# Kernel optimization log

Hardware: AMD Instinct MI355X
Metric: run time of the kernel (lower is better)

## Reference

```python
import jax, jax.numpy as jnp
import numpy as np

N_NODES = 50000
N_EDGES = 800000
D_IN = 128
D_OUT = 128


def setup_inputs() -> dict:
    key = jax.random.key(0)
    k = jax.random.split(key, 6)
    x = jax.random.normal(k[0], (N_NODES, D_IN), dtype=jnp.float32)
    weight = jax.random.normal(k[1], (D_IN, D_OUT), dtype=jnp.float32) * (1.0 / np.sqrt(D_IN))
    bias = jax.random.normal(k[2], (D_OUT,), dtype=jnp.float32)
    src = jax.random.randint(k[3], (N_EDGES,), 0, N_NODES, dtype=jnp.int32)
    dst = jax.random.randint(k[4], (N_EDGES,), 0, N_NODES, dtype=jnp.int32)
    edge_vals = jax.random.uniform(k[5], (N_EDGES,), dtype=jnp.float32)
    return {"x": x, "weight": weight, "bias": bias, "src": src, "dst": dst, "edge_vals": edge_vals}


def reference(x, weight, bias, src, dst, edge_vals):
    # support = x @ W  (dense projection), [N, D_OUT]
    support = jnp.matmul(x, weight)
    # spmm: out[d] = sum_{e: dst[e]==d} edge_vals[e] * support[src[e]]
    msgs = support[src] * edge_vals[:, None]  # [E, D_OUT]
    out = jax.ops.segment_sum(msgs, dst, num_segments=x.shape[0])
    return out + bias
```

## Files before the change

### kernel.cpp

```cpp
#include <hip/hip_runtime.h>
#include <hip/hip_bf16.h>

#define D 128
#define BKT 64
#define CAP 1536
#define SC_EPB 4096
#define NBMAX 800

typedef __attribute__((ext_vector_type(8))) short bf16x8;
typedef __attribute__((ext_vector_type(4))) float f32x4;

__device__ __forceinline__ unsigned short f2bf(float f) {
  union { float f; unsigned u; } c; c.f = f;
  unsigned u = c.u + 0x7FFFu + ((c.u >> 16) & 1u);
  return (unsigned short)(u >> 16);
}
__device__ __forceinline__ float bf_lo(unsigned u) {
  union { unsigned u; float f; } c; c.u = u << 16; return c.f;
}
__device__ __forceinline__ float bf_hi(unsigned u) {
  union { unsigned u; float f; } c; c.u = u & 0xFFFF0000u; return c.f;
}

__global__ __launch_bounds__(256) void setup(
    const float* __restrict__ w, unsigned short* __restrict__ wT,
    int* __restrict__ bcur, int nb) {
  const int idx = blockIdx.x * 256 + threadIdx.x;
  if (idx < D * D) {
    const int k = idx >> 7, n = idx & 127;
    wT[n * D + k] = f2bf(w[idx]);
  }
  if (idx < nb) bcur[idx] = 0;
}

__global__ __launch_bounds__(256) void gemm_xw_mfma(
    const float* __restrict__ x, const unsigned short* __restrict__ wT,
    unsigned short* __restrict__ supb, int n_nodes) {
  __shared__ unsigned short xs[64 * 136];

  const int tid = threadIdx.x;
  const int row0 = blockIdx.x * 64;

  for (int f = tid; f < 64 * 32; f += 256) {
    const int r = f >> 5, c4 = f & 31;
    const int gr = row0 + r;
    float4 v = make_float4(0.f, 0.f, 0.f, 0.f);
    if (gr < n_nodes) v = ((const float4*)(x + (size_t)gr * D))[c4];
    ushort4 b;
    b.x = f2bf(v.x); b.y = f2bf(v.y); b.z = f2bf(v.z); b.w = f2bf(v.w);
    *(ushort4*)(&xs[r * 136 + c4 * 4]) = b;
  }
  __syncthreads();

  const int wv = tid >> 6;
  const int lane = tid & 63;
  const int l15 = lane & 15;
  const int quad = lane >> 4;

  f32x4 acc[8];
#pragma unroll
  for (int t = 0; t < 8; t++) acc[t] = (f32x4){0.f, 0.f, 0.f, 0.f};

#pragma unroll
  for (int k0 = 0; k0 < D; k0 += 32) {
    const bf16x8 a = *(const bf16x8*)(&xs[(wv * 16 + l15) * 136 + k0 + quad * 8]);
    const unsigned short* wp = wT + (size_t)l15 * D + k0 + quad * 8;
#pragma unroll
    for (int t = 0; t < 8; t++) {
      const bf16x8 b = *(const bf16x8*)(wp + (size_t)t * 16 * D);
      acc[t] = __builtin_amdgcn_mfma_f32_16x16x32_bf16(a, b, acc[t], 0, 0, 0);
    }
  }

#pragma unroll
  for (int t = 0; t < 8; t++) {
    const int col = t * 16 + l15;
#pragma unroll
    for (int r = 0; r < 4; r++) {
      const int row = row0 + wv * 16 + quad * 4 + r;
      if (row < n_nodes) supb[(size_t)row * D + col] = f2bf(acc[t][r]);
    }
  }
}

__global__ __launch_bounds__(512) void bucket_scatter(
    const int* __restrict__ src, const int* __restrict__ dst,
    const float* __restrict__ ev, int* __restrict__ bcur,
    uint2* __restrict__ staged, int n_edges, int nb) {
  __shared__ int hist[NBMAX];
  __shared__ int cur[NBMAX];
  const int t = threadIdx.x;
  const int base = blockIdx.x * SC_EPB;
  const int cnt = min(SC_EPB, n_edges - base);

  for (int i = t; i < nb; i += 512) hist[i] = 0;
  __syncthreads();
  for (int j = t; j < cnt; j += 512) atomicAdd(&hist[dst[base + j] >> 6], 1);
  __syncthreads();
  for (int i = t; i < nb; i += 512) {
    const int h = hist[i];
    cur[i] = h ? atomicAdd(&bcur[i], h) : 0;
  }
  __syncthreads();
  for (int j = t; j < cnt; j += 512) {
    const int e = base + j;
    const int d = dst[e];
    const int b = d >> 6;
    const int p = atomicAdd(&cur[b], 1);
    if (p < CAP) {
      staged[(size_t)b * CAP + p] =
          make_uint2((unsigned)src[e] | ((unsigned)(d & 63) << 16),
                     (unsigned)__float_as_int(ev[e]));
    }
  }
}

__global__ __launch_bounds__(1024) void bucket_reduce(
    const unsigned short* __restrict__ supb, const uint2* __restrict__ staged,
    const int* __restrict__ bcnt, const float* __restrict__ bias,
    float* __restrict__ out, int n_nodes) {
  __shared__ uint2 rec[CAP];
  __shared__ uint2 ordered[CAP];
  __shared__ int hist[BKT];
  __shared__ int segbase[BKT];
  __shared__ int cur[BKT];

  const int t = threadIdx.x;
  const int b = blockIdx.x;
  const int lo = b << 6;
  const int cnt = min(bcnt[b], CAP);
  const uint2* st = staged + (size_t)b * CAP;

  if (t < BKT) hist[t] = 0;
  __syncthreads();
  for (int j = t; j < cnt; j += 1024) {
    const uint2 p = st[j];
    rec[j] = p;
    atomicAdd(&hist[p.x >> 16], 1);
  }
  __syncthreads();
  if (t < BKT) {
    const int h = hist[t];
    int incl = h;
#pragma unroll
    for (int ofs = 1; ofs < 64; ofs <<= 1) {
      const int v = __shfl_up(incl, ofs, 64);
      if (t >= ofs) incl += v;
    }
    segbase[t] = incl - h;
    cur[t] = incl - h;
  }
  __syncthreads();
  for (int j = t; j < cnt; j += 1024) {
    const uint2 p = rec[j];
    const int pos = atomicAdd(&cur[p.x >> 16], 1);
    ordered[pos] = p;
  }
  __syncthreads();

  const int n = t >> 4;
  const int p = t & 15;
  const int beg = segbase[n];
  const int end = beg + hist[n];

  float a[8];
#pragma unroll
  for (int k = 0; k < 8; k++) a[k] = 0.f;

  int j = beg;
  for (; j + 2 <= end; j += 2) {
    const uint2 pr0 = ordered[j];
    const uint2 pr1 = ordered[j + 1];
    const uint4 r0 = ((const uint4*)(supb + (size_t)(pr0.x & 0xFFFF) * D))[p];
    const uint4 r1 = ((const uint4*)(supb + (size_t)(pr1.x & 0xFFFF) * D))[p];
    const float v0 = __int_as_float((int)pr0.y);
    const float v1 = __int_as_float((int)pr1.y);
    a[0] += v0 * bf_lo(r0.x) + v1 * bf_lo(r1.x);
    a[1] += v0 * bf_hi(r0.x) + v1 * bf_hi(r1.x);
    a[2] += v0 * bf_lo(r0.y) + v1 * bf_lo(r1.y);
    a[3] += v0 * bf_hi(r0.y) + v1 * bf_hi(r1.y);
    a[4] += v0 * bf_lo(r0.z) + v1 * bf_lo(r1.z);
    a[5] += v0 * bf_hi(r0.z) + v1 * bf_hi(r1.z);
    a[6] += v0 * bf_lo(r0.w) + v1 * bf_lo(r1.w);
    a[7] += v0 * bf_hi(r0.w) + v1 * bf_hi(r1.w);
  }
  if (j < end) {
    const uint2 pr0 = ordered[j];
    const uint4 r0 = ((const uint4*)(supb + (size_t)(pr0.x & 0xFFFF) * D))[p];
    const float v0 = __int_as_float((int)pr0.y);
    a[0] += v0 * bf_lo(r0.x);
    a[1] += v0 * bf_hi(r0.x);
    a[2] += v0 * bf_lo(r0.y);
    a[3] += v0 * bf_hi(r0.y);
    a[4] += v0 * bf_lo(r0.z);
    a[5] += v0 * bf_hi(r0.z);
    a[6] += v0 * bf_lo(r0.w);
    a[7] += v0 * bf_hi(r0.w);
  }

  const int node = lo + n;
  if (node < n_nodes) {
    const float4 bv0 = ((const float4*)bias)[p * 2];
    const float4 bv1 = ((const float4*)bias)[p * 2 + 1];
    float4* op = (float4*)out + (size_t)node * 32 + p * 2;
    op[0] = make_float4(a[0] + bv0.x, a[1] + bv0.y, a[2] + bv0.z, a[3] + bv0.w);
    op[1] = make_float4(a[4] + bv1.x, a[5] + bv1.y, a[6] + bv1.z, a[7] + bv1.w);
  }
}

extern "C" void kernel_launch(void* const* d_in, const int* in_sizes, int n_in,
                              void* d_out, int out_size, void* d_ws, size_t ws_size,
                              hipStream_t stream) {
  const float* x    = (const float*)d_in[0];
  const float* w    = (const float*)d_in[1];
  const float* bias = (const float*)d_in[2];
  const int*   src  = (const int*)d_in[3];
  const int*   dst  = (const int*)d_in[4];
  const float* ev   = (const float*)d_in[5];
  float* out = (float*)d_out;

  const int n_nodes = in_sizes[0] / D;
  const int n_edges = in_sizes[3];
  const int nb = (n_nodes + BKT - 1) / BKT;

  unsigned short* supb = (unsigned short*)d_ws;
  unsigned short* wT = supb + (size_t)n_nodes * D;
  int* bcur = (int*)(wT + D * D);
  uint2* staged = (uint2*)(bcur + NBMAX);

  setup<<<64, 256, 0, stream>>>(w, wT, bcur, nb);

  bucket_scatter<<<(n_edges + SC_EPB - 1) / SC_EPB, 512, 0, stream>>>(
      src, dst, ev, bcur, staged, n_edges, nb);

  gemm_xw_mfma<<<(n_nodes + 63) / 64, 256, 0, stream>>>(x, wT, supb, n_nodes);

  bucket_reduce<<<nb, 1024, 0, stream>>>(supb, staged, bcur, bias, out, n_nodes);
}
```

Measured before the change: 153.0 us.

## Fuse edge bucket scatter and GEMM into one launch; unroll reduce by four

Merges the edge-bucketing scatter kernel and the bf16 MFMA projection GEMM into a single launch, with the block index range split between the two roles. The independent scatter and GEMM work can then run concurrently on the GPU, and one kernel launch and the idle gap between the two kernels disappear. GEMM blocks now hold two 64-row sub-tiles of 256 threads each, which doubles the block's shared memory. The reduce loop's gather is also unrolled from two to four edges per iteration to raise memory-level parallelism, at the cost of more registers.

```diff
diff --git a/kernel.cpp b/kernel.cpp
--- a/kernel.cpp
+++ b/kernel.cpp
@@ -33,84 +33,87 @@
   if (idx < nb) bcur[idx] = 0;
 }
 
-__global__ __launch_bounds__(256) void gemm_xw_mfma(
+__global__ __launch_bounds__(512) void fused_scatter_gemm(
     const float* __restrict__ x, const unsigned short* __restrict__ wT,
-    unsigned short* __restrict__ supb, int n_nodes) {
-  __shared__ unsigned short xs[64 * 136];
-
-  const int tid = threadIdx.x;
-  const int row0 = blockIdx.x * 64;
-
-  for (int f = tid; f < 64 * 32; f += 256) {
-    const int r = f >> 5, c4 = f & 31;
-    const int gr = row0 + r;
-    float4 v = make_float4(0.f, 0.f, 0.f, 0.f);
-    if (gr < n_nodes) v = ((const float4*)(x + (size_t)gr * D))[c4];
-    ushort4 b;
-    b.x = f2bf(v.x); b.y = f2bf(v.y); b.z = f2bf(v.z); b.w = f2bf(v.w);
-    *(ushort4*)(&xs[r * 136 + c4 * 4]) = b;
-  }
-  __syncthreads();
-
-  const int wv = tid >> 6;
-  const int lane = tid & 63;
-  const int l15 = lane & 15;
-  const int quad = lane >> 4;
-
-  f32x4 acc[8];
-#pragma unroll
-  for (int t = 0; t < 8; t++) acc[t] = (f32x4){0.f, 0.f, 0.f, 0.f};
-
-#pragma unroll
-  for (int k0 = 0; k0 < D; k0 += 32) {
-    const bf16x8 a = *(const bf16x8*)(&xs[(wv * 16 + l15) * 136 + k0 + quad * 8]);
-    const unsigned short* wp = wT + (size_t)l15 * D + k0 + quad * 8;
-#pragma unroll
-    for (int t = 0; t < 8; t++) {
-      const bf16x8 b = *(const bf16x8*)(wp + (size_t)t * 16 * D);
-      acc[t] = __builtin_amdgcn_mfma_f32_16x16x32_bf16(a, b, acc[t], 0, 0, 0);
-    }
-  }
-
-#pragma unroll
-  for (int t = 0; t < 8; t++) {
-    const int col = t * 16 + l15;
-#pragma unroll
-    for (int r = 0; r < 4; r++) {
-      const int row = row0 + wv * 16 + quad * 4 + r;
-      if (row < n_nodes) supb[(size_t)row * D + col] = f2bf(acc[t][r]);
-    }
-  }
-}
-
-__global__ __launch_bounds__(512) void bucket_scatter(
+    unsigned short* __restrict__ supb, int n_nodes,
     const int* __restrict__ src, const int* __restrict__ dst,
     const float* __restrict__ ev, int* __restrict__ bcur,
-    uint2* __restrict__ staged, int n_edges, int nb) {
-  __shared__ int hist[NBMAX];
-  __shared__ int cur[NBMAX];
+    uint2* __restrict__ staged, int n_edges, int nb, int gemm_blocks) {
+  __shared__ char smem[2 * 64 * 136 * 2];
   const int t = threadIdx.x;
-  const int base = blockIdx.x * SC_EPB;
-  const int cnt = min(SC_EPB, n_edges - base);
-
-  for (int i = t; i < nb; i += 512) hist[i] = 0;
-  __syncthreads();
-  for (int j = t; j < cnt; j += 512) atomicAdd(&hist[dst[base + j] >> 6], 1);
-  __syncthreads();
-  for (int i = t; i < nb; i += 512) {
-    const int h = hist[i];
-    cur[i] = h ? atomicAdd(&bcur[i], h) : 0;
-  }
-  __syncthreads();
-  for (int j = t; j < cnt; j += 512) {
-    const int e = base + j;
-    const int d = dst[e];
-    const int b = d >> 6;
-    const int p = atomicAdd(&cur[b], 1);
-    if (p < CAP) {
-      staged[(size_t)b * CAP + p] =
-          make_uint2((unsigned)src[e] | ((unsigned)(d & 63) << 16),
-                     (unsigned)__float_as_int(ev[e]));
+
+  if ((int)blockIdx.x < gemm_blocks) {
+    const int sub = t >> 8;
+    const int t256 = t & 255;
+    unsigned short* xs = (unsigned short*)smem + sub * (64 * 136);
+    const int row0 = blockIdx.x * 128 + sub * 64;
+
+    for (int f = t256; f < 64 * 32; f += 256) {
+      const int r = f >> 5, c4 = f & 31;
+      const int gr = row0 + r;
+      float4 v = make_float4(0.f, 0.f, 0.f, 0.f);
+      if (gr < n_nodes) v = ((const float4*)(x + (size_t)gr * D))[c4];
+      ushort4 b;
+      b.x = f2bf(v.x); b.y = f2bf(v.y); b.z = f2bf(v.z); b.w = f2bf(v.w);
+      *(ushort4*)(&xs[r * 136 + c4 * 4]) = b;
+    }
+    __syncthreads();
+
+    const int wv = t256 >> 6;
+    const int lane = t256 & 63;
+    const int l15 = lane & 15;
+    const int quad = lane >> 4;
+
+    f32x4 acc[8];
+#pragma unroll
+    for (int q = 0; q < 8; q++) acc[q] = (f32x4){0.f, 0.f, 0.f, 0.f};
+
+#pragma unroll
+    for (int k0 = 0; k0 < D; k0 += 32) {
+      const bf16x8 a =
+          *(const bf16x8*)(&xs[(wv * 16 + l15) * 136 + k0 + quad * 8]);
+      const unsigned short* wp = wT + (size_t)l15 * D + k0 + quad * 8;
+#pragma unroll
+      for (int q = 0; q < 8; q++) {
+        const bf16x8 b = *(const bf16x8*)(wp + (size_t)q * 16 * D);
+        acc[q] = __builtin_amdgcn_mfma_f32_16x16x32_bf16(a, b, acc[q], 0, 0, 0);
+      }
+    }
+
+#pragma unroll
+    for (int q = 0; q < 8; q++) {
+      const int col = q * 16 + l15;
+#pragma unroll
+      for (int r = 0; r < 4; r++) {
+        const int row = row0 + wv * 16 + quad * 4 + r;
+        if (row < n_nodes) supb[(size_t)row * D + col] = f2bf(acc[q][r]);
+      }
+    }
+  } else {
+    int* hist = (int*)smem;
+    int* cur = hist + NBMAX;
+    const int base = ((int)blockIdx.x - gemm_blocks) * SC_EPB;
+    const int cnt = min(SC_EPB, n_edges - base);
+
+    for (int i = t; i < nb; i += 512) hist[i] = 0;
+    __syncthreads();
+    for (int j = t; j < cnt; j += 512) atomicAdd(&hist[dst[base + j] >> 6], 1);
+    __syncthreads();
+    for (int i = t; i < nb; i += 512) {
+      const int h = hist[i];
+      cur[i] = h ? atomicAdd(&bcur[i], h) : 0;
+    }
+    __syncthreads();
+    for (int j = t; j < cnt; j += 512) {
+      const int e = base + j;
+      const int d = dst[e];
+      const int b = d >> 6;
+      const int p = atomicAdd(&cur[b], 1);
+      if (p < CAP) {
+        staged[(size_t)b * CAP + p] =
+            make_uint2((unsigned)src[e] | ((unsigned)(d & 63) << 16),
+                       (unsigned)__float_as_int(ev[e]));
+      }
     }
   }
 }
@@ -168,23 +171,29 @@
   for (int k = 0; k < 8; k++) a[k] = 0.f;
 
   int j = beg;
-  for (; j + 2 <= end; j += 2) {
+  for (; j + 4 <= end; j += 4) {
     const uint2 pr0 = ordered[j];
     const uint2 pr1 = ordered[j + 1];
+    const uint2 pr2 = ordered[j + 2];
+    const uint2 pr3 = ordered[j + 3];
     const uint4 r0 = ((const uint4*)(supb + (size_t)(pr0.x & 0xFFFF) * D))[p];
     const uint4 r1 = ((const uint4*)(supb + (size_t)(pr1.x & 0xFFFF) * D))[p];
+    const uint4 r2 = ((const uint4*)(supb + (size_t)(pr2.x & 0xFFFF) * D))[p];
+    const uint4 r3 = ((const uint4*)(supb + (size_t)(pr3.x & 0xFFFF) * D))[p];
     const float v0 = __int_as_float((int)pr0.y);
     const float v1 = __int_as_float((int)pr1.y);
-    a[0] += v0 * bf_lo(r0.x) + v1 * bf_lo(r1.x);
-    a[1] += v0 * bf_hi(r0.x) + v1 * bf_hi(r1.x);
-    a[2] += v0 * bf_lo(r0.y) + v1 * bf_lo(r1.y);
-    a[3] += v0 * bf_hi(r0.y) + v1 * bf_hi(r1.y);
-    a[4] += v0 * bf_lo(r0.z) + v1 * bf_lo(r1.z);
-    a[5] += v0 * bf_hi(r0.z) + v1 * bf_hi(r1.z);
-    a[6] += v0 * bf_lo(r0.w) + v1 * bf_lo(r1.w);
-    a[7] += v0 * bf_hi(r0.w) + v1 * bf_hi(r1.w);
-  }
-  if (j < end) {
+    const float v2 = __int_as_float((int)pr2.y);
+    const float v3 = __int_as_float((int)pr3.y);
+    a[0] += v0 * bf_lo(r0.x) + v1 * bf_lo(r1.x) + v2 * bf_lo(r2.x) + v3 * bf_lo(r3.x);
+    a[1] += v0 * bf_hi(r0.x) + v1 * bf_hi(r1.x) + v2 * bf_hi(r2.x) + v3 * bf_hi(r3.x);
+    a[2] += v0 * bf_lo(r0.y) + v1 * bf_lo(r1.y) + v2 * bf_lo(r2.y) + v3 * bf_lo(r3.y);
+    a[3] += v0 * bf_hi(r0.y) + v1 * bf_hi(r1.y) + v2 * bf_hi(r2.y) + v3 * bf_hi(r3.y);
+    a[4] += v0 * bf_lo(r0.z) + v1 * bf_lo(r1.z) + v2 * bf_lo(r2.z) + v3 * bf_lo(r3.z);
+    a[5] += v0 * bf_hi(r0.z) + v1 * bf_hi(r1.z) + v2 * bf_hi(r2.z) + v3 * bf_hi(r3.z);
+    a[6] += v0 * bf_lo(r0.w) + v1 * bf_lo(r1.w) + v2 * bf_lo(r2.w) + v3 * bf_lo(r3.w);
+    a[7] += v0 * bf_hi(r0.w) + v1 * bf_hi(r1.w) + v2 * bf_hi(r2.w) + v3 * bf_hi(r3.w);
+  }
+  for (; j < end; j++) {
     const uint2 pr0 = ordered[j];
     const uint4 r0 = ((const uint4*)(supb + (size_t)(pr0.x & 0xFFFF) * D))[p];
     const float v0 = __int_as_float((int)pr0.y);
@@ -230,10 +239,11 @@
 
   setup<<<64, 256, 0, stream>>>(w, wT, bcur, nb);
 
-  bucket_scatter<<<(n_edges + SC_EPB - 1) / SC_EPB, 512, 0, stream>>>(
-      src, dst, ev, bcur, staged, n_edges, nb);
-
-  gemm_xw_mfma<<<(n_nodes + 63) / 64, 256, 0, stream>>>(x, wT, supb, n_nodes);
+  const int gemm_blocks = (n_nodes + 127) / 128;
+  const int scat_blocks = (n_edges + SC_EPB - 1) / SC_EPB;
+  fused_scatter_gemm<<<gemm_blocks + scat_blocks, 512, 0, stream>>>(
+      x, wT, supb, n_nodes, src, dst, ev, bcur, staged, n_edges, nb,
+      gemm_blocks);
 
   bucket_reduce<<<nb, 1024, 0, stream>>>(supb, staged, bcur, bias, out, n_nodes);
 }
```

Result: faster. 144.0 us (-5.8%).
